# Kernel tuning notes

Hardware: AMD Instinct MI355X
Metric: run time of the kernel (lower is better)

Reference implementation:

```python
import jax, jax.numpy as jnp
import numpy as np

C, G, S, L, B = 16, 8192, 8, 3, 32


def setup_inputs() -> dict:
    key = jax.random.key(0)
    kx, kI = jax.random.split(key)
    # x: valuation vector over G ground atoms per batch element, in [0,1)
    x = jax.random.uniform(kx, (B, G), dtype=jnp.float32)
    # I: precomputed index tensor [C, G, S, L], indices into the G axis of x
    I = jax.random.randint(kI, (C, G, S, L), 0, G, dtype=jnp.int64)
    return {"x": x, "I": I}


def reference(x, I):
    # Equivalent of: for each clause i, gather(V_tild, 1, I_i) -> prod over L -> sum over S
    # torch gather semantics: out[b, g, s, l] = x[b, I[i, g, s, l]]
    # Vectorized over all clauses at once; no repeat/broadcast materialization beyond the gather.
    gathered = x[:, I]                        # [B, C, G, S, L]
    body = jnp.prod(gathered, axis=-1)        # conjunction over L body literals -> [B, C, G, S]
    clause_val = jnp.sum(body, axis=-1)       # sum over S substitutions -> [B, C, G]
    # torch.stack over clauses puts C first: [C, B, G]
    return jnp.transpose(clause_val, (1, 0, 2))
```

## Files before the change

kernel.cpp:

```cpp
#include <hip/hip_runtime.h>

#define Cc 16
#define Gg 8192
#define Ss 8
#define Ll 3
#define Bb 32

#define SLICES 16
#define GTILE 64
#define THREADS 512

__global__ __launch_bounds__(256) void build_xpairs(const float* __restrict__ x,
                                                    float2* __restrict__ xs) {
    int t = blockIdx.x * 256 + threadIdx.x;
    int z = t >> 13;
    int g = t & (Gg - 1);
    float a = x[(size_t)(2 * z) * Gg + g];
    float b = x[(size_t)(2 * z + 1) * Gg + g];
    xs[t] = make_float2(a, b);
}

__global__ __launch_bounds__(THREADS, 4) void clause_kernel(const float2* __restrict__ xs,
                                                            const int* __restrict__ I,
                                                            float* __restrict__ out) {
    __shared__ float2 xl[Gg];
    const int tid = threadIdx.x;
    const int z = blockIdx.y;
    const int g0 = blockIdx.x * GTILE;

    const float4* src = (const float4*)(xs + (size_t)z * Gg);
    float4* dst = (float4*)xl;
    #pragma unroll
    for (int i = 0; i < 8; ++i)
        dst[tid + i * THREADS] = src[tid + i * THREADS];
    __syncthreads();

    #pragma unroll
    for (int it = 0; it < 2; ++it) {
        int w = it * THREADS + tid;
        int c = w >> 6;
        int gl = w & 63;
        int g = g0 + gl;

        const int4* I4 = (const int4*)(I + ((size_t)c * Gg + g) * (Ss * Ll));
        int4 q0 = I4[0], q1 = I4[1], q2 = I4[2], q3 = I4[3], q4 = I4[4], q5 = I4[5];
        int idx[Ss * Ll] = {q0.x, q0.y, q0.z, q0.w, q1.x, q1.y, q1.z, q1.w,
                            q2.x, q2.y, q2.z, q2.w, q3.x, q3.y, q3.z, q3.w,
                            q4.x, q4.y, q4.z, q4.w, q5.x, q5.y, q5.z, q5.w};

        float2 v[Ss * Ll];
        #pragma unroll
        for (int k = 0; k < Ss * Ll; ++k)
            v[k] = xl[idx[k]];

        float2 s = {0.f, 0.f};
        #pragma unroll
        for (int q = 0; q < Ss; ++q) {
            s.x += v[3 * q].x * v[3 * q + 1].x * v[3 * q + 2].x;
            s.y += v[3 * q].y * v[3 * q + 1].y * v[3 * q + 2].y;
        }

        float* op = out + ((size_t)(c * Bb + 2 * z)) * Gg + g;
        op[0] = s.x;
        op[Gg] = s.y;
    }
}

__global__ __launch_bounds__(256) void clause_kernel_direct(const float* __restrict__ x,
                                                            const int* __restrict__ I,
                                                            float* __restrict__ out) {
    const int tid = threadIdx.x;
    const int b = tid & 31;
    const int j = tid >> 5;
    const int g = blockIdx.x * 8 + j;
    const int c = blockIdx.y;

    const int* Icg = I + (size_t)(c * Gg + g) * (Ss * Ll);
    float sum = 0.f;
    #pragma unroll
    for (int s = 0; s < Ss; ++s) {
        float p0 = x[(size_t)b * Gg + Icg[3 * s + 0]];
        float p1 = x[(size_t)b * Gg + Icg[3 * s + 1]];
        float p2 = x[(size_t)b * Gg + Icg[3 * s + 2]];
        sum += p0 * p1 * p2;
    }
    out[(size_t)(c * Bb + b) * Gg + g] = sum;
}

extern "C" void kernel_launch(void* const* d_in, const int* in_sizes, int n_in,
                              void* d_out, int out_size, void* d_ws, size_t ws_size,
                              hipStream_t stream) {
    const float* x = (const float*)d_in[0];
    const int* I = (const int*)d_in[1];
    float* out = (float*)d_out;

    const size_t xs_bytes = (size_t)SLICES * Gg * sizeof(float2);

    if (ws_size >= xs_bytes) {
        float2* xs = (float2*)d_ws;
        build_xpairs<<<(SLICES * Gg) / 256, 256, 0, stream>>>(x, xs);
        clause_kernel<<<dim3(Gg / GTILE, SLICES), THREADS, 0, stream>>>(xs, I, out);
    } else {
        clause_kernel_direct<<<dim3(Gg / 8, Cc), 256, 0, stream>>>(x, I, out);
    }
}
```

Before: 83.81 us.

## Loop all batch slices per block with double-buffered async LDS staging

Each block now owns 512 (clause, ground-atom) pairs and loops over all 16 batch-pair slices. The index tensor is therefore read once per pair instead of once per slice. The x slices are staged into a double-buffered 128KB LDS region with global_load_lds async copies, prefetching the next slice while the current one is gathered. In exchange, the grid shrinks to 256 blocks with one block per CU, which lowers occupancy and adds more total LDS fill traffic per block. Correctness also relies on the barrier waiting for the async loads to finish.

```diff
diff --git a/kernel.cpp b/kernel.cpp
--- a/kernel.cpp
+++ b/kernel.cpp
@@ -7,8 +7,27 @@
 #define Bb 32
 
 #define SLICES 16
-#define GTILE 64
 #define THREADS 512
+
+__device__ __forceinline__ void async_load16(const void* gsrc, void* lds) {
+    uint32_t l32 = (uint32_t)__builtin_amdgcn_readfirstlane((uint32_t)(uintptr_t)lds);
+    __builtin_amdgcn_global_load_lds(
+        (const __attribute__((address_space(1))) uint32_t*)(uintptr_t)gsrc,
+        (__attribute__((address_space(3))) uint32_t*)(uintptr_t)l32,
+        16, 0, 0);
+}
+
+__device__ __forceinline__ void stage_slice(const float2* gsrc, float2* ldst, int tid) {
+    const char* g = (const char*)gsrc;
+    char* l = (char*)ldst;
+    const int lane = tid & 63;
+    const int w = tid >> 6;
+    #pragma unroll
+    for (int i = 0; i < 8; ++i) {
+        int off = ((i << 3) | w) << 10;
+        async_load16(g + off + lane * 16, l + off);
+    }
+}
 
 __global__ __launch_bounds__(256) void build_xpairs(const float* __restrict__ x,
                                                     float2* __restrict__ xs) {
@@ -20,38 +39,36 @@
     xs[t] = make_float2(a, b);
 }
 
-__global__ __launch_bounds__(THREADS, 4) void clause_kernel(const float2* __restrict__ xs,
-                                                            const int* __restrict__ I,
-                                                            float* __restrict__ out) {
-    __shared__ float2 xl[Gg];
+__global__ __launch_bounds__(THREADS) void clause_all(const float2* __restrict__ xs,
+                                                      const int* __restrict__ I,
+                                                      float* __restrict__ out) {
+    __shared__ float2 buf[2 * Gg];
     const int tid = threadIdx.x;
-    const int z = blockIdx.y;
-    const int g0 = blockIdx.x * GTILE;
+    const int flat = blockIdx.x * THREADS + tid;
+    const int c = flat >> 13;
+    const int g = flat & (Gg - 1);
 
-    const float4* src = (const float4*)(xs + (size_t)z * Gg);
-    float4* dst = (float4*)xl;
-    #pragma unroll
-    for (int i = 0; i < 8; ++i)
-        dst[tid + i * THREADS] = src[tid + i * THREADS];
-    __syncthreads();
+    stage_slice(xs, buf, tid);
 
-    #pragma unroll
-    for (int it = 0; it < 2; ++it) {
-        int w = it * THREADS + tid;
-        int c = w >> 6;
-        int gl = w & 63;
-        int g = g0 + gl;
+    const int4* I4 = (const int4*)(I + ((size_t)c * Gg + g) * (Ss * Ll));
+    int4 q0 = I4[0], q1 = I4[1], q2 = I4[2], q3 = I4[3], q4 = I4[4], q5 = I4[5];
+    int idx[Ss * Ll] = {q0.x, q0.y, q0.z, q0.w, q1.x, q1.y, q1.z, q1.w,
+                        q2.x, q2.y, q2.z, q2.w, q3.x, q3.y, q3.z, q3.w,
+                        q4.x, q4.y, q4.z, q4.w, q5.x, q5.y, q5.z, q5.w};
 
-        const int4* I4 = (const int4*)(I + ((size_t)c * Gg + g) * (Ss * Ll));
-        int4 q0 = I4[0], q1 = I4[1], q2 = I4[2], q3 = I4[3], q4 = I4[4], q5 = I4[5];
-        int idx[Ss * Ll] = {q0.x, q0.y, q0.z, q0.w, q1.x, q1.y, q1.z, q1.w,
-                            q2.x, q2.y, q2.z, q2.w, q3.x, q3.y, q3.z, q3.w,
-                            q4.x, q4.y, q4.z, q4.w, q5.x, q5.y, q5.z, q5.w};
+    float* op = out + ((size_t)(c * Bb)) * Gg + g;
+
+    #pragma unroll 1
+    for (int z = 0; z < SLICES; ++z) {
+        __syncthreads();
+        float2* cur = buf + (z & 1) * Gg;
+        if (z + 1 < SLICES)
+            stage_slice(xs + (size_t)(z + 1) * Gg, buf + ((z + 1) & 1) * Gg, tid);
 
         float2 v[Ss * Ll];
         #pragma unroll
         for (int k = 0; k < Ss * Ll; ++k)
-            v[k] = xl[idx[k]];
+            v[k] = cur[idx[k]];
 
         float2 s = {0.f, 0.f};
         #pragma unroll
@@ -60,9 +77,8 @@
             s.y += v[3 * q].y * v[3 * q + 1].y * v[3 * q + 2].y;
         }
 
-        float* op = out + ((size_t)(c * Bb + 2 * z)) * Gg + g;
-        op[0] = s.x;
-        op[Gg] = s.y;
+        op[(size_t)(2 * z) * Gg] = s.x;
+        op[(size_t)(2 * z + 1) * Gg] = s.y;
     }
 }
 
@@ -99,7 +115,7 @@
     if (ws_size >= xs_bytes) {
         float2* xs = (float2*)d_ws;
         build_xpairs<<<(SLICES * Gg) / 256, 256, 0, stream>>>(x, xs);
-        clause_kernel<<<dim3(Gg / GTILE, SLICES), THREADS, 0, stream>>>(xs, I, out);
+        clause_all<<<(Cc * Gg) / THREADS, THREADS, 0, stream>>>(xs, I, out);
     } else {
         clause_kernel_direct<<<dim3(Gg / 8, Cc), 256, 0, stream>>>(x, I, out);
     }
```

Result: slower. 91.52 us (+9.2%).
